# Optimization experiments

Measured on AMD Instinct MI355X. Metric: run time of the kernel, lower is better.

## Reference

```python
import jax, jax.numpy as jnp
import numpy as np
import math

# ---- config (matches init_kwargs / Mamba defaults) ----
B_SZ = 16
IMG = 224
PATCH = 16
D_MODEL = 384
DEPTH = 24
D_INNER = 2 * D_MODEL          # expand=2
D_STATE = 16
D_CONV = 4
DT_RANK = math.ceil(D_MODEL / D_STATE)
N_CLASSES = 1000
L_TOK = (IMG // PATCH) ** 2     # 196

C_CURV = 0.5
SQRT_C = math.sqrt(C_CURV)
MAX_NORM = 0.95 / SQRT_C

# ---- StablePoincareBall ops ----
def _norm(x):
    return jnp.sqrt(jnp.sum(x * x, axis=-1, keepdims=True) + 1e-15)

def expmap0(u):
    n = jnp.clip(_norm(u), 1e-8, 5.0)
    res = jnp.tanh(SQRT_C * n) / SQRT_C * (u / n)
    rn = _norm(res)
    scale = jnp.where(rn > MAX_NORM, MAX_NORM / rn, jnp.ones_like(rn))
    return res * scale

def logmap0(y):
    n = jnp.clip(_norm(y), 1e-8, MAX_NORM)
    return jnp.arctanh(jnp.minimum(SQRT_C * n, 0.95)) / SQRT_C * (y / n)

def mobius_add(a, b):
    xy = jnp.sum(a * b, -1, keepdims=True)
    x2 = jnp.sum(a * a, -1, keepdims=True)
    y2 = jnp.sum(b * b, -1, keepdims=True)
    num = (1 + 2 * C_CURV * xy + C_CURV * y2) * a + (1 - C_CURV * x2) * b
    den = 1 + 2 * C_CURV * xy + (C_CURV ** 2) * x2 * y2
    return num / jnp.maximum(den, 1e-15)

def mobius_matvec(M, x):
    xn = jnp.maximum(_norm(x), 1e-8)
    mx = x @ M.T
    mxn = jnp.maximum(_norm(mx), 1e-8)
    t = jnp.tanh(mxn / xn * jnp.arctanh(jnp.minimum(SQRT_C * xn, 1.0 - 1e-5)))
    return t * mx / (mxn * SQRT_C)

def hyp_layernorm(x, gamma, beta, eps=1e-5):
    t = logmap0(x)
    mean = t.mean(-1, keepdims=True)
    # torch .std() is unbiased (ddof=1)
    var = jnp.sum((t - mean) ** 2, -1, keepdims=True) / (t.shape[-1] - 1)
    tn = (t - mean) / (jnp.sqrt(var) + eps)
    return expmap0(tn * gamma + beta)

def silu(x):
    return x * jax.nn.sigmoid(x)

# ---- Mamba selective scan (recompute dA per step; carry only h) ----
def selective_scan(u, dt, A, Bm, Cm):
    # u, dt: (B,L,Din); A: (Din,N); Bm, Cm: (B,L,N)
    def step(h, inp):
        dt_t, B_t, C_t, u_t = inp              # (B,Din),(B,N),(B,N),(B,Din)
        dA = jnp.exp(dt_t[..., None] * A)      # (B,Din,N)
        h = dA * h + dt_t[..., None] * B_t[:, None, :] * u_t[..., None]
        y = jnp.sum(h * C_t[:, None, :], -1)   # (B,Din)
        return h, y
    h0 = jnp.zeros((u.shape[0], u.shape[2], A.shape[1]), u.dtype)
    _, ys = jax.lax.scan(step, h0, (dt.transpose(1, 0, 2), Bm.transpose(1, 0, 2),
                                    Cm.transpose(1, 0, 2), u.transpose(1, 0, 2)))
    return ys.transpose(1, 0, 2)               # (B,L,Din)

def mamba_mixer(x, in_w, cw, cb, xp_w, dt_w, dt_b, A_log, Dp, out_w):
    xz = x @ in_w.T                            # (B,L,2*Din)
    xc, z = xz[..., :D_INNER], xz[..., D_INNER:]
    xt = xc.transpose(0, 2, 1)                 # (B,Din,L)
    xpad = jnp.pad(xt, ((0, 0), (0, 0), (D_CONV - 1, 0)))
    L = xt.shape[-1]
    conv = sum(cw[:, k][None, :, None] * xpad[:, :, k:k + L] for k in range(D_CONV))
    conv = conv + cb[None, :, None]
    u = silu(conv.transpose(0, 2, 1))          # (B,L,Din)
    dbl = u @ xp_w.T                           # (B,L,dt_rank+2N)
    dt_r = dbl[..., :DT_RANK]
    Bm = dbl[..., DT_RANK:DT_RANK + D_STATE]
    Cm = dbl[..., DT_RANK + D_STATE:]
    dt = jax.nn.softplus(dt_r @ dt_w.T + dt_b)
    A = -jnp.exp(A_log)
    y = selective_scan(u, dt, A, Bm, Cm) + Dp * u
    y = y * silu(z)
    return y @ out_w.T


def setup_inputs() -> dict:
    key = jax.random.key(0)
    ks = jax.random.split(key, 24)
    f32 = jnp.float32
    inp = {}
    inp['x'] = jax.random.normal(ks[0], (B_SZ, 3, IMG, IMG), f32)
    inp['patch_w'] = jax.random.normal(ks[1], (D_MODEL, 3, PATCH, PATCH), f32) * 0.02
    inp['patch_b'] = jax.random.normal(ks[2], (D_MODEL,), f32) * 0.005
    inp['hyp_w'] = jax.random.normal(ks[3], (D_MODEL, D_MODEL), f32) * (1.0 / math.sqrt(D_MODEL))
    inp['hyp_b'] = jax.random.normal(ks[4], (D_MODEL,), f32) * 0.01
    inp['pe_gamma'] = jnp.ones((D_MODEL,), f32)
    inp['pe_beta'] = jnp.zeros((D_MODEL,), f32)
    inp['pos_embed'] = jax.random.normal(ks[5], (1, L_TOK, D_MODEL), f32) * 0.02
    inp['in_proj_w'] = jax.random.normal(ks[6], (DEPTH, 2 * D_INNER, D_MODEL), f32) * 0.02
    inp['conv_w'] = jax.random.normal(ks[7], (DEPTH, D_INNER, D_CONV), f32) * 0.1
    inp['conv_b'] = jnp.zeros((DEPTH, D_INNER), f32)
    inp['x_proj_w'] = jax.random.normal(ks[8], (DEPTH, DT_RANK + 2 * D_STATE, D_INNER), f32) * 0.02
    inp['dt_proj_w'] = jax.random.normal(ks[9], (DEPTH, D_INNER, DT_RANK), f32) * (1.0 / math.sqrt(DT_RANK))
    inp['dt_proj_b'] = jnp.log(jnp.expm1(jnp.full((DEPTH, D_INNER), 0.01, f32)))  # dt init ~0.01
    inp['A_log'] = jnp.tile(jnp.log(jnp.arange(1, D_STATE + 1, dtype=f32))[None, None, :], (DEPTH, D_INNER, 1))
    inp['Dp'] = jnp.ones((DEPTH, D_INNER), f32)
    inp['out_proj_w'] = jax.random.normal(ks[10], (DEPTH, D_MODEL, D_INNER), f32) * (0.02 / math.sqrt(DEPTH))
    inp['gamma'] = jnp.ones((DEPTH, D_MODEL), f32)
    inp['beta'] = jnp.zeros((DEPTH, D_MODEL), f32)
    inp['gamma_f'] = jnp.ones((D_MODEL,), f32)
    inp['beta_f'] = jnp.zeros((D_MODEL,), f32)
    inp['prototypes'] = expmap0(jax.random.normal(ks[11], (N_CLASSES, D_MODEL), f32) * 0.1)
    return inp


def reference(x, patch_w, patch_b, hyp_w, hyp_b, pe_gamma, pe_beta, pos_embed,
              in_proj_w, conv_w, conv_b, x_proj_w, dt_proj_w, dt_proj_b,
              A_log, Dp, out_proj_w, gamma, beta, gamma_f, beta_f, prototypes):
    # patch embed conv
    feat = jax.lax.conv_general_dilated(x, patch_w, (PATCH, PATCH), 'VALID',
                                        dimension_numbers=('NCHW', 'OIHW', 'NCHW'))
    feat = feat + patch_b[None, :, None, None]
    B, D, Hp, Wp = feat.shape
    tokens = feat.reshape(B, D, Hp * Wp).transpose(0, 2, 1)   # (B,L,D)
    h = expmap0(tokens)
    h = mobius_add(mobius_matvec(hyp_w, h), hyp_b)
    h = hyp_layernorm(h, pe_gamma, pe_beta)
    h = expmap0(logmap0(h) + pos_embed)                        # tangent-space pos add
    hidden, residual = h, None
    for i in range(DEPTH):
        residual = hidden if residual is None else hidden + residual
        hn = hyp_layernorm(residual, gamma[i], beta[i])
        hidden = mamba_mixer(hn, in_proj_w[i], conv_w[i], conv_b[i], x_proj_w[i],
                             dt_proj_w[i], dt_proj_b[i], A_log[i], Dp[i], out_proj_w[i])
    residual = hidden + residual
    hf = hyp_layernorm(residual, gamma_f, beta_f)
    pooled = expmap0(logmap0(hf).mean(axis=1))                 # tangent mean pool
    # hyperbolic distance head: logits = -dist(x, prototypes)
    diff = mobius_add(-pooled[:, None, :], prototypes[None])
    dn = jnp.minimum(SQRT_C * _norm(diff)[..., 0], 1.0 - 1e-5)
    return -(2.0 / SQRT_C) * jnp.arctanh(dn)                   # (B, num_classes)
```

## Files before the change

### kernel.cpp

```cpp
#include <hip/hip_runtime.h>
#include <hip/hip_bf16.h>
#include <math.h>

#define D_MODEL 384
#define D_INNER 768
#define D_STATE 16
#define DT_RANK 24
#define NXP 56
#define LTOK 196
#define BSZ 16
#define NROW 3136
#define NDEPTH 24
#define NCLS 1000

constexpr float kSqrtC   = 0.70710678118654752440f;
constexpr float kMaxNorm = 0.95f / 0.70710678118654752440f;

typedef unsigned short u16;
typedef short  bf16x8 __attribute__((ext_vector_type(8)));
typedef u16    u16x8  __attribute__((ext_vector_type(8)));
typedef float  f32x4  __attribute__((ext_vector_type(4)));

__device__ __forceinline__ float clampf(float x, float lo, float hi) {
  return fminf(fmaxf(x, lo), hi);
}

__device__ __forceinline__ u16 f2bf(float f) {
  union { float f; unsigned u; } v; v.f = f;
  return (u16)((v.u + 0x7FFFu + ((v.u >> 16) & 1u)) >> 16);
}
__device__ __forceinline__ float bf2f(u16 s) {
  union { unsigned u; float f; } v; v.u = ((unsigned)s) << 16;
  return v.f;
}

__device__ __forceinline__ void gload16(const u16* g, u16* l) {
  __builtin_amdgcn_global_load_lds(
      (const __attribute__((address_space(1))) unsigned int*)g,
      (__attribute__((address_space(3))) unsigned int*)l, 16, 0, 0);
}

__device__ __forceinline__ float fsig(float x) {
  return __fdividef(1.f, 1.f + __expf(-x));
}
__device__ __forceinline__ float fsilu(float x) { return x * fsig(x); }
__device__ __forceinline__ float fsoftplus(float x) {
  return (x > 20.f) ? x : __logf(1.f + __expf(x));
}
__device__ __forceinline__ float ftanh(float x) {
  float e = __expf(2.f * x);
  return __fdividef(e - 1.f, e + 1.f);
}
__device__ __forceinline__ float fatanh(float x) {
  return 0.5f * __logf(__fdividef(1.f + x, 1.f - x));
}

__device__ __forceinline__ float waveSum(float v) {
#pragma unroll
  for (int o = 1; o < 64; o <<= 1) v += __shfl_xor(v, o, 64);
  return v;
}

__device__ __forceinline__ float blockSum128(float v, float* sm) {
#pragma unroll
  for (int o = 32; o > 0; o >>= 1) v += __shfl_down(v, o, 64);
  __syncthreads();
  if ((threadIdx.x & 63) == 0) sm[threadIdx.x >> 6] = v;
  __syncthreads();
  return sm[0] + sm[1];
}

__global__ __launch_bounds__(256) void k_cvt5(
    const float* __restrict__ s0, u16* __restrict__ d0, int n0,
    const float* __restrict__ s1, u16* __restrict__ d1, int n1,
    const float* __restrict__ s2, u16* __restrict__ d2, int n2,
    const float* __restrict__ s3, u16* __restrict__ d3, int n3,
    const float* __restrict__ s4, u16* __restrict__ d4, int n4) {
  int i = blockIdx.x * 256 + threadIdx.x;
  const float* s; u16* d;
  if (i < n0) { s = s0; d = d0; }
  else if ((i -= n0) < n1) { s = s1; d = d1; }
  else if ((i -= n1) < n2) { s = s2; d = d2; }
  else if ((i -= n2) < n3) { s = s3; d = d3; }
  else if ((i -= n3) < n4) { s = s4; d = d4; }
  else return;
  float4 v = ((const float4*)s)[i];
  short4 o = {(short)f2bf(v.x), (short)f2bf(v.y), (short)f2bf(v.z),
              (short)f2bf(v.w)};
  *(short4*)&d[(size_t)i * 4] = o;
}

__global__ __launch_bounds__(256) void k_im2col(const float* __restrict__ x,
                                                u16* __restrict__ P) {
  size_t idx = (size_t)blockIdx.x * 256 + threadIdx.x;
  if (idx >= (size_t)NROW * 768) return;
  int k = (int)(idx % 768);
  int r = (int)(idx / 768);
  int b = r / LTOK, t = r % LTOK;
  int hp = t / 14, wp = t % 14;
  int c = k / 256, rem = k % 256, i = rem / 16, j = rem % 16;
  P[idx] = f2bf(
      x[(((size_t)(b * 3 + c) * 224) + hp * 16 + i) * 224 + wp * 16 + j]);
}

__global__ __launch_bounds__(256) void k_gemm_bb(
    const u16* __restrict__ A, const u16* __restrict__ W,
    const float* __restrict__ bias, void* __restrict__ Cn,
    void* __restrict__ Ct, int K, int lda, int ldc, int ldct, int Nv, int act,
    int obf, int obf_t) {
  __shared__ u16 As[2][64 * 64];
  __shared__ u16 Ws[2][64 * 64];
  const int tid = threadIdx.x;
  const int m0 = blockIdx.x * 64;
  const int n0 = blockIdx.y * 64;
  const int lane = tid & 63;
  const int w = tid >> 6;
  const int wm = w & 1, wn = w >> 1;
  const int lm = lane & 15;
  const int quad = lane >> 4;
  const int r8 = lane >> 3;
  const int t8 = lane & 7;
  const int gsg = t8 ^ r8;
  const int s = lm & 7;

  f32x4 acc[2][2];
#pragma unroll
  for (int i = 0; i < 2; i++)
#pragma unroll
    for (int j = 0; j < 2; j++) acc[i][j] = (f32x4){0.f, 0.f, 0.f, 0.f};

  auto stage = [&](int buf, int k0) {
#pragma unroll
    for (int cc = 0; cc < 2; cc++) {
      const int c = 2 * w + cc;
      const int row = c * 8 + r8;
      gload16(A + (size_t)(m0 + row) * lda + k0 + gsg * 8, &As[buf][c * 512]);
      gload16(W + (size_t)(n0 + row) * K + k0 + gsg * 8, &Ws[buf][c * 512]);
    }
  };
  stage(0, 0);
  __syncthreads();
  int cur = 0;
  for (int k0 = 0; k0 < K; k0 += 64) {
    if (k0 + 64 < K) stage(cur ^ 1, k0 + 64);
#pragma unroll
    for (int h = 0; h < 2; h++) {
      const int col = (((h << 2) + quad) ^ s) << 3;
      bf16x8 af[2], bfr[2];
#pragma unroll
      for (int i = 0; i < 2; i++) {
        af[i]  = *(bf16x8*)&As[cur][(wm * 32 + i * 16 + lm) * 64 + col];
        bfr[i] = *(bf16x8*)&Ws[cur][(wn * 32 + i * 16 + lm) * 64 + col];
      }
#pragma unroll
      for (int i = 0; i < 2; i++)
#pragma unroll
        for (int j = 0; j < 2; j++)
          acc[i][j] = __builtin_amdgcn_mfma_f32_16x16x32_bf16(
              af[i], bfr[j], acc[i][j], 0, 0, 0);
    }
    __syncthreads();
    cur ^= 1;
  }
#pragma unroll
  for (int i = 0; i < 2; i++) {
#pragma unroll
    for (int j = 0; j < 2; j++) {
      int cg = n0 + wn * 32 + j * 16 + lm;
      if (cg >= Nv) continue;
      float bj = bias ? bias[cg] : 0.f;
      float o[4];
      int rgb = m0 + wm * 32 + i * 16 + quad * 4;
#pragma unroll
      for (int reg = 0; reg < 4; reg++) {
        float v = acc[i][j][reg] + bj;
        if (act == 1) v = fsoftplus(v);
        else if (act == 2 && cg >= 768) v = fsilu(v);
        o[reg] = v;
      }
      if (Cn) {
#pragma unroll
        for (int reg = 0; reg < 4; reg++) {
          if (obf) ((u16*)Cn)[(size_t)(rgb + reg) * ldc + cg] = f2bf(o[reg]);
          else ((float*)Cn)[(size_t)(rgb + reg) * ldc + cg] = o[reg];
        }
      }
      if (Ct) {
        if (obf_t) {
          short4 o4 = {(short)f2bf(o[0]), (short)f2bf(o[1]), (short)f2bf(o[2]),
                       (short)f2bf(o[3])};
          *(short4*)&((u16*)Ct)[(size_t)cg * ldct + rgb] = o4;
        } else {
          float4 o4 = {o[0], o[1], o[2], o[3]};
          *(float4*)&((float*)Ct)[(size_t)cg * ldct + rgb] = o4;
        }
      }
    }
  }
}

__global__ __launch_bounds__(256) void k_gemm_n128(
    const u16* __restrict__ A, const u16* __restrict__ W,
    u16* __restrict__ Cx, u16* __restrict__ Zt, int K, int lda, int ldc) {
  __shared__ u16 As[2][64 * 64];
  __shared__ u16 Ws[2][128 * 64];
  const int tid = threadIdx.x;
  const int m0 = blockIdx.x * 64;
  const int n0 = blockIdx.y * 128;
  const int lane = tid & 63;
  const int w = tid >> 6;
  const int lm = lane & 15;
  const int quad = lane >> 4;
  const int r8 = lane >> 3;
  const int t8 = lane & 7;
  const int gsg = t8 ^ r8;
  const int s = lm & 7;

  f32x4 acc[4][2];
#pragma unroll
  for (int i = 0; i < 4; i++)
#pragma unroll
    for (int j = 0; j < 2; j++) acc[i][j] = (f32x4){0.f, 0.f, 0.f, 0.f};

  auto stage = [&](int buf, int k0) {
#pragma unroll
    for (int cc = 0; cc < 2; cc++) {
      const int c = 2 * w + cc;
      gload16(A + (size_t)(m0 + c * 8 + r8) * lda + k0 + gsg * 8,
              &As[buf][c * 512]);
    }
#pragma unroll
    for (int cc = 0; cc < 4; cc++) {
      const int c = 4 * w + cc;
      gload16(W + (size_t)(n0 + c * 8 + r8) * K + k0 + gsg * 8,
              &Ws[buf][c * 512]);
    }
  };
  stage(0, 0);
  __syncthreads();
  int cur = 0;
  for (int k0 = 0; k0 < K; k0 += 64) {
    if (k0 + 64 < K) stage(cur ^ 1, k0 + 64);
#pragma unroll
    for (int h = 0; h < 2; h++) {
      const int col = (((h << 2) + quad) ^ s) << 3;
      bf16x8 af[4], bfr[2];
#pragma unroll
      for (int i = 0; i < 4; i++)
        af[i] = *(bf16x8*)&As[cur][(i * 16 + lm) * 64 + col];
#pragma unroll
      for (int j = 0; j < 2; j++)
        bfr[j] = *(bf16x8*)&Ws[cur][(w * 32 + j * 16 + lm) * 64 + col];
#pragma unroll
      for (int i = 0; i < 4; i++)
#pragma unroll
        for (int j = 0; j < 2; j++)
          acc[i][j] = __builtin_amdgcn_mfma_f32_16x16x32_bf16(
              af[i], bfr[j], acc[i][j], 0, 0, 0);
    }
    __syncthreads();
    cur ^= 1;
  }
#pragma unroll
  for (int i = 0; i < 4; i++) {
#pragma unroll
    for (int j = 0; j < 2; j++) {
      int cg = n0 + w * 32 + j * 16 + lm;
      int rgb = m0 + i * 16 + quad * 4;
      if (cg < 768) {
#pragma unroll
        for (int reg = 0; reg < 4; reg++)
          Cx[(size_t)(rgb + reg) * ldc + cg] = f2bf(acc[i][j][reg]);
      } else {
        short4 o4 = {(short)f2bf(fsilu(acc[i][j][0])),
                     (short)f2bf(fsilu(acc[i][j][1])),
                     (short)f2bf(fsilu(acc[i][j][2])),
                     (short)f2bf(fsilu(acc[i][j][3]))};
        *(short4*)&Zt[(size_t)(cg - 768) * NROW + rgb] = o4;
      }
    }
  }
}

__global__ __launch_bounds__(128) void k_stem_a(const float* __restrict__ tok,
                                                u16* __restrict__ hb,
                                                float* __restrict__ xn) {
  __shared__ float sm[2];
  const int r = blockIdx.x, tid = threadIdx.x;
  float v[3];
#pragma unroll
  for (int j = 0; j < 3; j++) v[j] = tok[(size_t)r * D_MODEL + tid + j * 128];
  float s = blockSum128(v[0] * v[0] + v[1] * v[1] + v[2] * v[2], sm);
  float n = sqrtf(s + 1e-15f);
  float nc = clampf(n, 1e-8f, 5.f);
  float ke = tanhf(kSqrtC * nc) / (kSqrtC * nc);
  float rn = sqrtf(ke * ke * s + 1e-15f);
  float sc = rn > kMaxNorm ? kMaxNorm / rn : 1.f;
  float kk = ke * sc;
#pragma unroll
  for (int j = 0; j < 3; j++)
    hb[(size_t)r * D_MODEL + tid + j * 128] = f2bf(kk * v[j]);
  if (tid == 0) xn[r] = fmaxf(sqrtf(kk * kk * s + 1e-15f), 1e-8f);
}

__global__ __launch_bounds__(128) void k_stem_b(
    const float* __restrict__ mx, const float* __restrict__ xn,
    const float* __restrict__ hyp_b, const float* __restrict__ pe_g,
    const float* __restrict__ pe_b, const float* __restrict__ pos,
    float* __restrict__ outh) {
  __shared__ float sm[2];
  const int r = blockIdx.x, tid = threadIdx.x;
  const int t = r % LTOK;
  float mv[3], bv[3];
  int dd[3];
#pragma unroll
  for (int j = 0; j < 3; j++) {
    dd[j] = tid + j * 128;
    mv[j] = mx[(size_t)r * D_MODEL + dd[j]];
    bv[j] = hyp_b[dd[j]];
  }
  float smx = blockSum128(mv[0] * mv[0] + mv[1] * mv[1] + mv[2] * mv[2], sm);
  float mxn = fmaxf(sqrtf(smx + 1e-15f), 1e-8f);
  float xnv = xn[r];
  float tt = tanhf(mxn / xnv * atanhf(fminf(kSqrtC * xnv, 1.f - 1e-5f)));
  float kres = tt / (mxn * kSqrtC);
  float res[3];
#pragma unroll
  for (int j = 0; j < 3; j++) res[j] = kres * mv[j];
  float xy = blockSum128(res[0] * bv[0] + res[1] * bv[1] + res[2] * bv[2], sm);
  float y2 = blockSum128(bv[0] * bv[0] + bv[1] * bv[1] + bv[2] * bv[2], sm);
  float x2 = kres * kres * smx;
  float al = 1.f + xy + 0.5f * y2;
  float be = 1.f - 0.5f * x2;
  float den = fmaxf(1.f + xy + 0.25f * x2 * y2, 1e-15f);
  float h1[3];
#pragma unroll
  for (int j = 0; j < 3; j++) h1[j] = (al * res[j] + be * bv[j]) / den;
  float s1 = blockSum128(h1[0] * h1[0] + h1[1] * h1[1] + h1[2] * h1[2], sm);
  float n1 = sqrtf(s1 + 1e-15f);
  float nc1 = clampf(n1, 1e-8f, kMaxNorm);
  float kl = atanhf(fminf(kSqrtC * nc1, 0.95f)) / (kSqrtC * nc1);
  float tl[3];
#pragma unroll
  for (int j = 0; j < 3; j++) tl[j] = kl * h1[j];
  float mean = blockSum128(tl[0] + tl[1] + tl[2], sm) * (1.f / 384.f);
  float dv = 0.f;
#pragma unroll
  for (int j = 0; j < 3; j++) { float d = tl[j] - mean; dv += d * d; }
  float var = blockSum128(dv, sm) * (1.f / 383.f);
  float inv = 1.f / (sqrtf(var) + 1e-5f);
  float g[3];
#pragma unroll
  for (int j = 0; j < 3; j++)
    g[j] = (tl[j] - mean) * inv * pe_g[dd[j]] + pe_b[dd[j]];
  float sg = blockSum128(g[0] * g[0] + g[1] * g[1] + g[2] * g[2], sm);
  float ng = sqrtf(sg + 1e-15f);
  float nc2 = clampf(ng, 1e-8f, 5.f);
  float ke = tanhf(kSqrtC * nc2) / (kSqrtC * nc2);
  float rn = sqrtf(ke * ke * sg + 1e-15f);
  float sc = rn > kMaxNorm ? kMaxNorm / rn : 1.f;
  float kk = ke * sc;
  float s2 = kk * kk * sg;
  float n3 = sqrtf(s2 + 1e-15f);
  float nc3 = clampf(n3, 1e-8f, kMaxNorm);
  float kl2 = atanhf(fminf(kSqrtC * nc3, 0.95f)) / (kSqrtC * nc3);
  float v[3];
#pragma unroll
  for (int j = 0; j < 3; j++)
    v[j] = kl2 * kk * g[j] + pos[(size_t)t * D_MODEL + dd[j]];
  float sv = blockSum128(v[0] * v[0] + v[1] * v[1] + v[2] * v[2], sm);
  float nv = sqrtf(sv + 1e-15f);
  float nc4 = clampf(nv, 1e-8f, 5.f);
  float ke2 = tanhf(kSqrtC * nc4) / (kSqrtC * nc4);
  float rn2 = sqrtf(ke2 * ke2 * sv + 1e-15f);
  float sc2 = rn2 > kMaxNorm ? kMaxNorm / rn2 : 1.f;
#pragma unroll
  for (int j = 0; j < 3; j++)
    outh[(size_t)r * D_MODEL + dd[j]] = ke2 * sc2 * v[j];
}

__global__ __launch_bounds__(256) void k_resln(
    const float* __restrict__ hid, const float* __restrict__ res_in,
    float* __restrict__ res_out, const float* __restrict__ g_,
    const float* __restrict__ b_, u16* __restrict__ out_bf,
    float* __restrict__ out_f, int first, int out_logmap) {
  const int lane = threadIdx.x & 63;
  const int r = blockIdx.x * 4 + (threadIdx.x >> 6);
  float v[6];
  int dd[6];
#pragma unroll
  for (int j = 0; j < 6; j++) {
    dd[j] = lane + j * 64;
    size_t idx = (size_t)r * D_MODEL + dd[j];
    v[j] = hid[idx] + (first ? 0.f : res_in[idx]);
    res_out[idx] = v[j];
  }
  float ss = 0.f;
#pragma unroll
  for (int j = 0; j < 6; j++) ss += v[j] * v[j];
  float s = waveSum(ss);
  float n = sqrtf(s + 1e-15f);
  float nc = clampf(n, 1e-8f, kMaxNorm);
  float kl = fatanh(fminf(kSqrtC * nc, 0.95f)) / (kSqrtC * nc);
  float t[6];
  float ts = 0.f;
#pragma unroll
  for (int j = 0; j < 6; j++) { t[j] = kl * v[j]; ts += t[j]; }
  float mean = waveSum(ts) * (1.f / 384.f);
  float dv = 0.f;
#pragma unroll
  for (int j = 0; j < 6; j++) { float d = t[j] - mean; dv += d * d; }
  float var = waveSum(dv) * (1.f / 383.f);
  float inv = 1.f / (sqrtf(var) + 1e-5f);
  float g[6];
  float gs = 0.f;
#pragma unroll
  for (int j = 0; j < 6; j++) {
    g[j] = (t[j] - mean) * inv * g_[dd[j]] + b_[dd[j]];
    gs += g[j] * g[j];
  }
  float sg = waveSum(gs);
  float ng = sqrtf(sg + 1e-15f);
  float nc2 = clampf(ng, 1e-8f, 5.f);
  float ke = ftanh(kSqrtC * nc2) / (kSqrtC * nc2);
  float rn = sqrtf(ke * ke * sg + 1e-15f);
  float sc = rn > kMaxNorm ? kMaxNorm / rn : 1.f;
  float kk = ke * sc;
  if (!out_logmap) {
#pragma unroll
    for (int j = 0; j < 6; j++)
      out_bf[(size_t)r * D_MODEL + dd[j]] = f2bf(kk * g[j]);
  } else {
    float s2 = kk * kk * sg;
    float n3 = sqrtf(s2 + 1e-15f);
    float nc3 = clampf(n3, 1e-8f, kMaxNorm);
    float kl2 = fatanh(fminf(kSqrtC * nc3, 0.95f)) / (kSqrtC * nc3);
#pragma unroll
    for (int j = 0; j < 6; j++)
      out_f[(size_t)r * D_MODEL + dd[j]] = kl2 * kk * g[j];
  }
}

__global__ __launch_bounds__(256) void k_convt(const u16* __restrict__ xc,
                                               const float* __restrict__ cw,
                                               const float* __restrict__ cb,
                                               u16* __restrict__ ut,
                                               u16* __restrict__ un) {
  __shared__ u16 sx[52][68];
  __shared__ u16 su2[49][68];
  const int d0 = blockIdx.x * 64;
  const int l0 = blockIdx.y * 49;
  const int b = blockIdx.z;
  const int t = threadIdx.x;
#pragma unroll
  for (int i = 0; i < 4; i++) {
    int idx = t + i * 256;
    if (idx < 832) {
      int row = idx >> 4, seg = idx & 15;
      int l = l0 - 3 + row;
      short4 v = {0, 0, 0, 0};
      if (l >= 0) {
        const u16* p = xc + (size_t)(b * LTOK + l) * D_INNER + d0 + seg * 4;
        v = *(const short4*)p;
      }
      *(short4*)&sx[row][seg * 4] = v;
    }
  }
  __syncthreads();
  const int dl = t & 63, lg = t >> 6;
  const int d = d0 + dl;
  const float c0 = cw[d * 4], c1 = cw[d * 4 + 1], c2 = cw[d * 4 + 2],
              c3 = cw[d * 4 + 3];
  const float bb = cb[d];
  for (int l = lg; l < 49; l += 4) {
    float acc = bb;
    acc = fmaf(c0, bf2f(sx[l + 0][dl]), acc);
    acc = fmaf(c1, bf2f(sx[l + 1][dl]), acc);
    acc = fmaf(c2, bf2f(sx[l + 2][dl]), acc);
    acc = fmaf(c3, bf2f(sx[l + 3][dl]), acc);
    su2[l][dl] = f2bf(fsilu(acc));
  }
  __syncthreads();
#pragma unroll
  for (int i = 0; i < 13; i++) {
    int idx = t + i * 256;
    if (idx < 3136) {
      int d_ = idx / 49, l_ = idx % 49;
      ut[(size_t)(d0 + d_) * NROW + b * LTOK + l0 + l_] = su2[l_][d_];
    }
  }
#pragma unroll
  for (int i = 0; i < 13; i++) {
    int idx = t + i * 256;
    if (idx < 3136) {
      int l_ = idx >> 6, d_ = idx & 63;
      un[(size_t)(b * LTOK + l0 + l_) * D_INNER + d0 + d_] = su2[l_][d_];
    }
  }
}

__global__ __launch_bounds__(256) void k_pscan(
    const u16* __restrict__ ut, const float* __restrict__ dblt,
    const float* __restrict__ dt_w, const float* __restrict__ dt_bias,
    const float* __restrict__ A_log, const float* __restrict__ Dp,
    const u16* __restrict__ zt, u16* __restrict__ yf) {
  __shared__ float2 sdu[4][196];
  __shared__ float sprod[196][18];
  const int d0 = blockIdx.x * 4, b = blockIdx.y;
  const int t = threadIdx.x;
  const size_t col0 = (size_t)b * LTOK;
  u16 zz[4] = {0, 0, 0, 0};
  float uo[4];
  if (t < 196) {
    float r[DT_RANK];
#pragma unroll
    for (int k = 0; k < DT_RANK; k++)
      r[k] = dblt[(size_t)k * NROW + col0 + t];
#pragma unroll
    for (int g = 0; g < 4; g++) {
      const int d = d0 + g;
      float acc = dt_bias[d];
#pragma unroll
      for (int k = 0; k < DT_RANK; k++)
        acc = fmaf(r[k], dt_w[d * DT_RANK + k], acc);
      float uv = bf2f(ut[(size_t)d * NROW + col0 + t]);
      sdu[g][t] = make_float2(fsoftplus(acc), uv);
      uo[g] = uv;
      zz[g] = zt[(size_t)d * NROW + col0 + t];
    }
  }
  const int c = t & 15, n = t >> 4;
  const bool act = c < 14;
  float Breg[14], Creg[14];
  if (act) {
    const float2* Bp =
        (const float2*)(dblt + (size_t)(DT_RANK + n) * NROW + col0 + c * 14);
    const float2* Cp = (const float2*)(
        dblt + (size_t)(DT_RANK + D_STATE + n) * NROW + col0 + c * 14);
#pragma unroll
    for (int j = 0; j < 7; j++) {
      float2 bv = Bp[j], cv = Cp[j];
      Breg[2 * j] = bv.x; Breg[2 * j + 1] = bv.y;
      Creg[2 * j] = cv.x; Creg[2 * j + 1] = cv.y;
    }
  }
  __syncthreads();
  u16 og[4];
#pragma unroll
  for (int g = 0; g < 4; g++) {
    const int d = d0 + g;
    const float a = -__expf(A_log[(size_t)d * D_STATE + n]);
    float dA[14], hh[14];
    float A = 1.f, Bc = 0.f;
    if (act) {
      float2 du[14];
#pragma unroll
      for (int j = 0; j < 14; j++) du[j] = sdu[g][c * 14 + j];
      float h = 0.f, p = 1.f;
#pragma unroll
      for (int j = 0; j < 14; j++) {
        float dtv = du[j].x;
        float e = __expf(dtv * a);
        h = fmaf(e, h, dtv * Breg[j] * du[j].y);
        dA[j] = e;
        hh[j] = h;
        p *= e;
      }
      A = p;
      Bc = h;
    }
#pragma unroll
    for (int off = 1; off < 16; off <<= 1) {
      float pA = __shfl_up(A, off, 16);
      float pB = __shfl_up(Bc, off, 16);
      if (c >= off) {
        Bc = fmaf(A, pB, Bc);
        A *= pA;
      }
    }
    float h0 = __shfl_up(Bc, 1, 16);
    if (c == 0) h0 = 0.f;
    if (g > 0) __syncthreads();
    if (act) {
      float p = 1.f;
#pragma unroll
      for (int j = 0; j < 14; j++) {
        p *= dA[j];
        sprod[c * 14 + j][n] = fmaf(p, h0, hh[j]) * Creg[j];
      }
    }
    __syncthreads();
    if (t < 196) {
      float y = 0.f;
#pragma unroll
      for (int pp = 0; pp < 8; pp++) {
        float2 v = *(float2*)&sprod[t][2 * pp];
        y += v.x;
        y += v.y;
      }
      float yv = bf2f(f2bf(fmaf(Dp[d], uo[g], y)));
      og[g] = f2bf(yv * bf2f(zz[g]));
    }
  }
  if (t < 196) {
    short4 o4 = {(short)og[0], (short)og[1], (short)og[2], (short)og[3]};
    *(short4*)&yf[(col0 + t) * D_INNER + d0] = o4;
  }
}

__global__ __launch_bounds__(128) void k_pool1(const float* __restrict__ tl,
                                               float* __restrict__ partial) {
  const int b = blockIdx.x, g = blockIdx.y, tid = threadIdx.x;
  float m[3] = {0.f, 0.f, 0.f};
  for (int l = g * 14; l < (g + 1) * 14; l++) {
    size_t row = ((size_t)b * LTOK + l) * D_MODEL;
#pragma unroll
    for (int j = 0; j < 3; j++) m[j] += tl[row + tid + j * 128];
  }
#pragma unroll
  for (int j = 0; j < 3; j++)
    partial[((size_t)b * 14 + g) * D_MODEL + tid + j * 128] = m[j];
}

__global__ __launch_bounds__(128) void k_pool2(const float* __restrict__ partial,
                                               float* __restrict__ pooled,
                                               float* __restrict__ x2v) {
  __shared__ float sm[2];
  const int b = blockIdx.x, tid = threadIdx.x;
  float m[3] = {0.f, 0.f, 0.f};
  for (int g = 0; g < 14; g++) {
    size_t row = ((size_t)b * 14 + g) * D_MODEL;
#pragma unroll
    for (int j = 0; j < 3; j++) m[j] += partial[row + tid + j * 128];
  }
#pragma unroll
  for (int j = 0; j < 3; j++) m[j] *= (1.f / (float)LTOK);
  float s = blockSum128(m[0] * m[0] + m[1] * m[1] + m[2] * m[2], sm);
  float n = sqrtf(s + 1e-15f);
  float nc = clampf(n, 1e-8f, 5.f);
  float ke = tanhf(kSqrtC * nc) / (kSqrtC * nc);
  float rn = sqrtf(ke * ke * s + 1e-15f);
  float sc = rn > kMaxNorm ? kMaxNorm / rn : 1.f;
  float kk = ke * sc;
  float p[3];
#pragma unroll
  for (int j = 0; j < 3; j++) {
    p[j] = kk * m[j];
    pooled[(size_t)b * D_MODEL + tid + j * 128] = p[j];
  }
  float s2 = blockSum128(p[0] * p[0] + p[1] * p[1] + p[2] * p[2], sm);
  if (tid == 0) x2v[b] = s2;
}

__global__ __launch_bounds__(256) void k_head(const float* __restrict__ pooled,
                                              const float* __restrict__ protos,
                                              const float* __restrict__ x2v,
                                              float* __restrict__ out) {
  __shared__ float sp[D_MODEL];
  const int b = blockIdx.y;
  const int c = blockIdx.x * 256 + threadIdx.x;
  for (int j = threadIdx.x; j < D_MODEL; j += 256)
    sp[j] = pooled[(size_t)b * D_MODEL + j];
  __syncthreads();
  if (c >= NCLS) return;
  const float* pr = protos + (size_t)c * D_MODEL;
  float dotv = 0.f, y2 = 0.f;
  for (int k = 0; k < D_MODEL; k++) {
    float w = pr[k];
    dotv += sp[k] * w;
    y2 += w * w;
  }
  float x2 = x2v[b];
  float xy = -dotv;
  float al = 1.f + xy + 0.5f * y2;
  float be = 1.f - 0.5f * x2;
  float num2 = al * al * x2 + 2.f * al * be * xy + be * be * y2;
  float den = fmaxf(1.f + xy + 0.25f * x2 * y2, 1e-15f);
  float r2 = num2 / (den * den) + 1e-15f;
  float dn = fminf(kSqrtC * sqrtf(r2), 1.f - 1e-5f);
  out[(size_t)b * NCLS + c] = -(2.f / kSqrtC) * atanhf(dn);
}

extern "C" void kernel_launch(void* const* d_in, const int* in_sizes, int n_in,
                              void* d_out, int out_size, void* d_ws,
                              size_t ws_size, hipStream_t stream) {
  const float* x        = (const float*)d_in[0];
  const float* patch_w  = (const float*)d_in[1];
  const float* patch_b  = (const float*)d_in[2];
  const float* hyp_w    = (const float*)d_in[3];
  const float* hyp_b    = (const float*)d_in[4];
  const float* pe_gamma = (const float*)d_in[5];
  const float* pe_beta  = (const float*)d_in[6];
  const float* pos      = (const float*)d_in[7];
  const float* in_w     = (const float*)d_in[8];
  const float* conv_w   = (const float*)d_in[9];
  const float* conv_b   = (const float*)d_in[10];
  const float* xp_w     = (const float*)d_in[11];
  const float* dt_w     = (const float*)d_in[12];
  const float* dt_bias  = (const float*)d_in[13];
  const float* A_log    = (const float*)d_in[14];
  const float* Dp       = (const float*)d_in[15];
  const float* out_w    = (const float*)d_in[16];
  const float* gamma    = (const float*)d_in[17];
  const float* beta     = (const float*)d_in[18];
  const float* gamma_f  = (const float*)d_in[19];
  const float* beta_f   = (const float*)d_in[20];
  const float* protos   = (const float*)d_in[21];
  float* out = (float*)d_out;

  char* cur = (char*)d_ws;
  auto alloc = [&](size_t bytes) {
    char* p = cur;
    cur += (bytes + 255) & ~(size_t)255;
    return (void*)p;
  };
  float* hidden  = (float*)alloc((size_t)NROW * D_MODEL * 4);
  float* resid   = (float*)alloc((size_t)NROW * D_MODEL * 4);
  float* dblt    = (float*)alloc((size_t)64 * NROW * 4);
  float* fscr    = (float*)alloc((size_t)NROW * 768 * 4);
  float* xn      = (float*)alloc((size_t)NROW * 4);
  float* pooled  = (float*)alloc((size_t)BSZ * D_MODEL * 4);
  float* x2v     = (float*)alloc((size_t)BSZ * 4);
  float* partial = (float*)alloc((size_t)BSZ * 14 * D_MODEL * 4);
  u16* hn_bf  = (u16*)alloc((size_t)NROW * D_MODEL * 2);
  u16* xc_bf  = (u16*)alloc((size_t)NROW * D_INNER * 2);
  u16* zt     = (u16*)alloc((size_t)D_INNER * NROW * 2);
  u16* ut     = (u16*)alloc((size_t)D_INNER * NROW * 2);
  u16* u_bf   = (u16*)alloc((size_t)NROW * D_INNER * 2);
  u16* yf     = (u16*)alloc((size_t)NROW * D_INNER * 2);
  const size_t n_inw  = (size_t)NDEPTH * 2 * D_INNER * D_MODEL;
  const size_t n_outw = (size_t)NDEPTH * D_MODEL * D_INNER;
  const size_t n_xpw  = (size_t)NDEPTH * NXP * D_INNER;
  const size_t n_pw   = (size_t)D_MODEL * 768;
  const size_t n_hw   = (size_t)D_MODEL * D_MODEL;
  u16* in_wb  = (u16*)alloc(n_inw * 2);
  u16* out_wb = (u16*)alloc(n_outw * 2);
  u16* xp_wb  = (u16*)alloc(n_xpw * 2);
  u16* p_wb   = (u16*)alloc(n_pw * 2);
  u16* h_wb   = (u16*)alloc(n_hw * 2);
  u16* P_bf     = yf;
  float* tokens = fscr;
  float* mx     = fscr + (size_t)NROW * D_MODEL;
  float* hnf    = fscr;

  {
    const int c0 = (int)(n_inw / 4), c1 = (int)(n_outw / 4),
              c2 = (int)(n_xpw / 4), c3 = (int)(n_pw / 4),
              c4 = (int)(n_hw / 4);
    const int tot = c0 + c1 + c2 + c3 + c4;
    k_cvt5<<<dim3((tot + 255) / 256), dim3(256), 0, stream>>>(
        in_w, in_wb, c0, out_w, out_wb, c1, xp_w, xp_wb, c2, patch_w, p_wb,
        c3, hyp_w, h_wb, c4);
  }

  k_im2col<<<dim3((NROW * 768) / 256), dim3(256), 0, stream>>>(x, P_bf);
  k_gemm_bb<<<dim3(NROW / 64, 6), dim3(256), 0, stream>>>(
      P_bf, p_wb, patch_b, tokens, nullptr, 768, 768, D_MODEL, 0, D_MODEL, 0,
      0, 0);
  k_stem_a<<<dim3(NROW), dim3(128), 0, stream>>>(tokens, hn_bf, xn);
  k_gemm_bb<<<dim3(NROW / 64, 6), dim3(256), 0, stream>>>(
      hn_bf, h_wb, nullptr, mx, nullptr, D_MODEL, D_MODEL, D_MODEL, 0, D_MODEL,
      0, 0, 0);
  k_stem_b<<<dim3(NROW), dim3(128), 0, stream>>>(mx, xn, hyp_b, pe_gamma,
                                                 pe_beta, pos, hidden);
  for (int i = 0; i < NDEPTH; i++) {
    k_resln<<<dim3(NROW / 4), dim3(256), 0, stream>>>(
        hidden, resid, resid, gamma + (size_t)i * D_MODEL,
        beta + (size_t)i * D_MODEL, hn_bf, nullptr, i == 0 ? 1 : 0, 0);
    k_gemm_n128<<<dim3(NROW / 64, (2 * D_INNER) / 128), dim3(256), 0, stream>>>(
        hn_bf, in_wb + (size_t)i * 2 * D_INNER * D_MODEL, xc_bf, zt, D_MODEL,
        D_MODEL, D_INNER);
    k_convt<<<dim3(12, 4, BSZ), dim3(256), 0, stream>>>(
        xc_bf, conv_w + (size_t)i * D_INNER * 4, conv_b + (size_t)i * D_INNER,
        ut, u_bf);
    k_gemm_bb<<<dim3(NROW / 64, 1), dim3(256), 0, stream>>>(
        u_bf, xp_wb + (size_t)i * NXP * D_INNER, nullptr, nullptr, dblt,
        D_INNER, D_INNER, 0, NROW, NXP, 0, 0, 0);
    k_pscan<<<dim3(D_INNER / 4, BSZ), dim3(256), 0, stream>>>(
        ut, dblt, dt_w + (size_t)i * D_INNER * DT_RANK,
        dt_bias + (size_t)i * D_INNER, A_log + (size_t)i * D_INNER * D_STATE,
        Dp + (size_t)i * D_INNER, zt, yf);
    k_gemm_bb<<<dim3(NROW / 64, 6), dim3(256), 0, stream>>>(
        yf, out_wb + (size_t)i * D_MODEL * D_INNER, nullptr, hidden, nullptr,
        D_INNER, D_INNER, D_MODEL, 0, D_MODEL, 0, 0, 0);
  }
  k_resln<<<dim3(NROW / 4), dim3(256), 0, stream>>>(
      hidden, resid, resid, gamma_f, beta_f, nullptr, hnf, 0, 1);
  k_pool1<<<dim3(BSZ, 14), dim3(128), 0, stream>>>(hnf, partial);
  k_pool2<<<dim3(BSZ), dim3(128), 0, stream>>>(partial, pooled, x2v);
  k_head<<<dim3((NCLS + 255) / 256, BSZ), dim3(256), 0, stream>>>(pooled,
                                                                  protos, x2v,
                                                                  out);
}
```

Before: 2.037 ms.

## Split-K x_proj GEMM with reduction kernel and LDS-staged transposed z stores

Replaces the x_proj GEMM, which launched only NROW/64 blocks, with a split-K kernel over four K chunks of 192. Each chunk writes float partials, and a separate reduction kernel sums them into the dt/B/C buffer. This raises parallelism for a narrow-N GEMM at the cost of an extra launch and extra partial-buffer traffic. Separately, the in_proj GEMM now stages the silu(z) tile through LDS so the transposed z output is written with 16-byte coalesced stores instead of scattered short4 writes.

```diff
diff --git a/kernel.cpp b/kernel.cpp
--- a/kernel.cpp
+++ b/kernel.cpp
@@ -12,6 +12,7 @@
 #define NROW 3136
 #define NDEPTH 24
 #define NCLS 1000
+#define XKC 192
 
 constexpr float kSqrtC   = 0.70710678118654752440f;
 constexpr float kMaxNorm = 0.95f / 0.70710678118654752440f;
@@ -199,6 +200,89 @@
   }
 }
 
+__global__ __launch_bounds__(256) void k_xproj(const u16* __restrict__ A,
+                                               const u16* __restrict__ W,
+                                               float* __restrict__ part) {
+  __shared__ u16 As[2][64 * 64];
+  __shared__ u16 Ws[2][64 * 64];
+  const int tid = threadIdx.x;
+  const int m0 = blockIdx.x * 64;
+  const int kb = blockIdx.y * XKC;
+  const int lane = tid & 63;
+  const int w = tid >> 6;
+  const int wm = w & 1, wn = w >> 1;
+  const int lm = lane & 15;
+  const int quad = lane >> 4;
+  const int r8 = lane >> 3;
+  const int t8 = lane & 7;
+  const int gsg = t8 ^ r8;
+  const int s = lm & 7;
+
+  f32x4 acc[2][2];
+#pragma unroll
+  for (int i = 0; i < 2; i++)
+#pragma unroll
+    for (int j = 0; j < 2; j++) acc[i][j] = (f32x4){0.f, 0.f, 0.f, 0.f};
+
+  auto stage = [&](int buf, int k0) {
+#pragma unroll
+    for (int cc = 0; cc < 2; cc++) {
+      const int c = 2 * w + cc;
+      const int row = c * 8 + r8;
+      gload16(A + (size_t)(m0 + row) * 768 + kb + k0 + gsg * 8,
+              &As[buf][c * 512]);
+      gload16(W + (size_t)row * 768 + kb + k0 + gsg * 8, &Ws[buf][c * 512]);
+    }
+  };
+  stage(0, 0);
+  __syncthreads();
+  int cur = 0;
+  for (int k0 = 0; k0 < XKC; k0 += 64) {
+    if (k0 + 64 < XKC) stage(cur ^ 1, k0 + 64);
+#pragma unroll
+    for (int h = 0; h < 2; h++) {
+      const int col = (((h << 2) + quad) ^ s) << 3;
+      bf16x8 af[2], bfr[2];
+#pragma unroll
+      for (int i = 0; i < 2; i++) {
+        af[i]  = *(bf16x8*)&As[cur][(wm * 32 + i * 16 + lm) * 64 + col];
+        bfr[i] = *(bf16x8*)&Ws[cur][(wn * 32 + i * 16 + lm) * 64 + col];
+      }
+#pragma unroll
+      for (int i = 0; i < 2; i++)
+#pragma unroll
+        for (int j = 0; j < 2; j++)
+          acc[i][j] = __builtin_amdgcn_mfma_f32_16x16x32_bf16(
+              af[i], bfr[j], acc[i][j], 0, 0, 0);
+    }
+    __syncthreads();
+    cur ^= 1;
+  }
+  float* base = part + (size_t)blockIdx.y * NXP * NROW;
+#pragma unroll
+  for (int i = 0; i < 2; i++) {
+#pragma unroll
+    for (int j = 0; j < 2; j++) {
+      int cg = wn * 32 + j * 16 + lm;
+      if (cg >= NXP) continue;
+      int rgb = m0 + wm * 32 + i * 16 + quad * 4;
+      float4 o4 = {acc[i][j][0], acc[i][j][1], acc[i][j][2], acc[i][j][3]};
+      *(float4*)&base[(size_t)cg * NROW + rgb] = o4;
+    }
+  }
+}
+
+__global__ __launch_bounds__(256) void k_dred(const float* __restrict__ p,
+                                              float* __restrict__ o, int n4) {
+  int i = blockIdx.x * 256 + threadIdx.x;
+  if (i >= n4) return;
+  const float4* pp = (const float4*)p;
+  float4 a = pp[i], b = pp[i + n4], c = pp[i + 2 * n4], d = pp[i + 3 * n4];
+  float4 r = {((a.x + b.x) + c.x) + d.x, ((a.y + b.y) + c.y) + d.y,
+              ((a.z + b.z) + c.z) + d.z, ((a.w + b.w) + c.w) + d.w};
+  ((float4*)o)[i] = r;
+}
+
 __global__ __launch_bounds__(256) void k_gemm_n128(
     const u16* __restrict__ A, const u16* __restrict__ W,
     u16* __restrict__ Cx, u16* __restrict__ Zt, int K, int lda, int ldc) {
@@ -261,24 +345,37 @@
     __syncthreads();
     cur ^= 1;
   }
-#pragma unroll
-  for (int i = 0; i < 4; i++) {
-#pragma unroll
-    for (int j = 0; j < 2; j++) {
-      int cg = n0 + w * 32 + j * 16 + lm;
-      int rgb = m0 + i * 16 + quad * 4;
-      if (cg < 768) {
+  if (n0 < 768) {
+#pragma unroll
+    for (int i = 0; i < 4; i++) {
+#pragma unroll
+      for (int j = 0; j < 2; j++) {
+        int cg = n0 + w * 32 + j * 16 + lm;
+        int rgb = m0 + i * 16 + quad * 4;
 #pragma unroll
         for (int reg = 0; reg < 4; reg++)
           Cx[(size_t)(rgb + reg) * ldc + cg] = f2bf(acc[i][j][reg]);
-      } else {
-        short4 o4 = {(short)f2bf(fsilu(acc[i][j][0])),
-                     (short)f2bf(fsilu(acc[i][j][1])),
-                     (short)f2bf(fsilu(acc[i][j][2])),
-                     (short)f2bf(fsilu(acc[i][j][3]))};
-        *(short4*)&Zt[(size_t)(cg - 768) * NROW + rgb] = o4;
-      }
-    }
+      }
+    }
+  } else {
+    u16* tz = (u16*)As;
+#pragma unroll
+    for (int i = 0; i < 4; i++) {
+#pragma unroll
+      for (int j = 0; j < 2; j++) {
+        int cl = w * 32 + j * 16 + lm;
+        int rl = i * 16 + quad * 4;
+#pragma unroll
+        for (int reg = 0; reg < 4; reg++)
+          tz[cl * 64 + rl + reg] = f2bf(fsilu(acc[i][j][reg]));
+      }
+    }
+    __syncthreads();
+    const int cl = tid >> 1, hf = tid & 1;
+    size_t base = (size_t)(n0 - 768 + cl) * NROW + m0 + hf * 32;
+#pragma unroll
+    for (int q = 0; q < 4; q++)
+      *(u16x8*)&Zt[base + q * 8] = *(u16x8*)&tz[cl * 64 + hf * 32 + q * 8];
   }
 }
 
@@ -717,6 +814,7 @@
   float* hidden  = (float*)alloc((size_t)NROW * D_MODEL * 4);
   float* resid   = (float*)alloc((size_t)NROW * D_MODEL * 4);
   float* dblt    = (float*)alloc((size_t)64 * NROW * 4);
+  float* dblt4   = (float*)alloc((size_t)4 * NXP * NROW * 4);
   float* fscr    = (float*)alloc((size_t)NROW * 768 * 4);
   float* xn      = (float*)alloc((size_t)NROW * 4);
   float* pooled  = (float*)alloc((size_t)BSZ * D_MODEL * 4);
@@ -763,6 +861,7 @@
       0, 0, 0);
   k_stem_b<<<dim3(NROW), dim3(128), 0, stream>>>(mx, xn, hyp_b, pe_gamma,
                                                  pe_beta, pos, hidden);
+  const int nred4 = (NXP * NROW) / 4;
   for (int i = 0; i < NDEPTH; i++) {
     k_resln<<<dim3(NROW / 4), dim3(256), 0, stream>>>(
         hidden, resid, resid, gamma + (size_t)i * D_MODEL,
@@ -773,9 +872,10 @@
     k_convt<<<dim3(12, 4, BSZ), dim3(256), 0, stream>>>(
         xc_bf, conv_w + (size_t)i * D_INNER * 4, conv_b + (size_t)i * D_INNER,
         ut, u_bf);
-    k_gemm_bb<<<dim3(NROW / 64, 1), dim3(256), 0, stream>>>(
-        u_bf, xp_wb + (size_t)i * NXP * D_INNER, nullptr, nullptr, dblt,
-        D_INNER, D_INNER, 0, NROW, NXP, 0, 0, 0);
+    k_xproj<<<dim3(NROW / 64, 4), dim3(256), 0, stream>>>(
+        u_bf, xp_wb + (size_t)i * NXP * D_INNER, dblt4);
+    k_dred<<<dim3((nred4 + 255) / 256), dim3(256), 0, stream>>>(dblt4, dblt,
+                                                                nred4);
     k_pscan<<<dim3(D_INNER / 4, BSZ), dim3(256), 0, stream>>>(
         ut, dblt, dt_w + (size_t)i * D_INNER * DT_RANK,
         dt_bias + (size_t)i * D_INNER, A_log + (size_t)i * D_INNER * D_STATE,
```

Result: faster. 1.987 ms (-2.5%).
